# Performance work log

Hardware: AMD Instinct MI355X
Metric: run time of the kernel (lower is better)

Reference implementation:

```python
import jax, jax.numpy as jnp
import numpy as np

L = 16            # number_of_grid_levels
T = 524288        # max_hash_table_entries (2^19)
F = 2             # hash_table_feature_dim
MIN_RES = 16      # coarsest_resolution
MAX_RES = 2048    # finest_resolution
WIDTH = 64        # mlp_width
OUT = 3           # output_channels
N = 1048576       # number of 2D query points
PRIME_Y = np.uint32(2654435761)  # NGP spatial hash prime for dim 1 (dim 0 prime = 1)


def _resolutions():
    g = np.exp((np.log(MAX_RES) - np.log(MIN_RES)) / (L - 1))
    return np.floor(MIN_RES * g ** np.arange(L)).astype(np.float32)  # [L]


def setup_inputs() -> dict:
    key = jax.random.key(0)
    ks = jax.random.split(key, 6)
    x = jax.random.uniform(ks[0], (N, 2), dtype=jnp.float32)
    # NGP hash tables are initialized small uniform
    tables = jax.random.uniform(ks[1], (L, T, F), minval=-1e-4, maxval=1e-4, dtype=jnp.float32)
    def dense(k, fi, fo):
        return (jax.random.normal(k, (fi, fo), dtype=jnp.float32) / np.sqrt(fi).astype(np.float32))
    W0 = dense(ks[2], L * F, WIDTH)
    W1 = dense(ks[3], WIDTH, WIDTH)
    W2 = dense(ks[4], WIDTH, OUT)
    return dict(x=x, tables=tables,
                W0=W0, b0=jnp.zeros((WIDTH,), jnp.float32),
                W1=W1, b1=jnp.zeros((WIDTH,), jnp.float32),
                W2=W2, b2=jnp.zeros((OUT,), jnp.float32))


def _hash_encode(x, tables):
    # Multi-resolution hash grid encoding (Instant-NGP, spatial_dim=2).
    res = jnp.asarray(_resolutions())                  # [L]
    scaled = x[:, None, :] * res[None, :, None]        # [N, L, 2]
    floored = jnp.floor(scaled)
    frac = scaled - floored                            # [N, L, 2]
    corners = jnp.array([[0, 0], [1, 0], [0, 1], [1, 1]], dtype=jnp.int32)  # [4, 2]
    vert = floored.astype(jnp.int32)[:, :, None, :] + corners[None, None]   # [N, L, 4, 2]
    vu = vert.astype(jnp.uint32)
    h = vu[..., 0] ^ (vu[..., 1] * PRIME_Y)            # spatial hash (prime for dim0 is 1)
    idx = (h % jnp.uint32(T)).astype(jnp.int32)        # [N, L, 4]
    feats = tables[jnp.arange(L)[None, :, None], idx]  # [N, L, 4, F] gather per level
    # bilinear weights: prod over dims of frac (if corner==1) else 1-frac
    wd = jnp.where(corners[None, None] == 1, frac[:, :, None, :], 1.0 - frac[:, :, None, :])
    w = wd[..., 0] * wd[..., 1]                        # [N, L, 4]
    interp = jnp.einsum('nlc,nlcf->nlf', w, feats)     # [N, L, F]
    return interp.reshape(x.shape[0], L * F)           # [N, L*F]


def reference(x, tables, W0, b0, W1, b1, W2, b2):
    h = _hash_encode(x, tables)
    h = jax.nn.relu(h @ W0 + b0)
    h = jax.nn.relu(h @ W1 + b1)
    return jax.nn.sigmoid(h @ W2 + b2)   # [N, 3]
```

## Files before the change

kernel.cpp:

```cpp
#include <hip/hip_runtime.h>

#define LVLS  16
#define TSZ   524288u
#define TMASK (TSZ - 1u)
#define PRIME 2654435761u

__constant__ float RES[LVLS] = {16.f, 22.f, 30.f, 42.f, 58.f, 80.f, 111.f, 153.f,
                                212.f, 294.f, 406.f, 561.f, 776.f, 1072.f, 1482.f, 2048.f};

typedef __bf16 bf16x8 __attribute__((ext_vector_type(8)));
typedef float  f32x4  __attribute__((ext_vector_type(4)));

union Frag {
    uint4          q;
    unsigned       u[4];
    unsigned short s[8];
    bf16x8         v;
};

static __device__ __forceinline__ unsigned short f2bf(float f) {
    unsigned u = __float_as_uint(f);
    u += 0x7FFFu + ((u >> 16) & 1u);
    return (unsigned short)(u >> 16);
}
static __device__ __forceinline__ unsigned pack2(float a, float b) {
    return (unsigned)f2bf(a) | ((unsigned)f2bf(b) << 16);
}
static __device__ __forceinline__ void lds_fence() {
    asm volatile("s_waitcnt lgkmcnt(0)" ::: "memory");
}

__global__ __launch_bounds__(256) void ngp_encode(
    const float* __restrict__ x, const float* __restrict__ tables,
    unsigned* __restrict__ feat, int N, int PB)
{
    const int g  = blockIdx.x;
    const int r  = g & 7;
    const int i  = g >> 3;
    const int hi = (i >= PB);
    const int l  = r + (hi << 3);
    const int pb = i - (hi ? PB : 0);
    const int n  = pb * 256 + threadIdx.x;
    if (n >= N) return;

    const float2 xy = ((const float2*)x)[n];
    const float res = RES[l];
    const float sx = xy.x * res, sy = xy.y * res;
    const float fx = floorf(sx),  fy = floorf(sy);
    const float ux = sx - fx,     uy = sy - fy;
    const unsigned ix = (unsigned)(int)fx, iy = (unsigned)(int)fy;
    const unsigned hy0 = iy * PRIME, hy1 = (iy + 1u) * PRIME;
    const unsigned i00 = (ix ^ hy0) & TMASK;
    const unsigned i10 = ((ix + 1u) ^ hy0) & TMASK;
    const unsigned i01 = (ix ^ hy1) & TMASK;
    const unsigned i11 = ((ix + 1u) ^ hy1) & TMASK;
    const float2* tb = (const float2*)(tables + (size_t)l * (TSZ * 2));
    const float2 f00 = tb[i00], f10 = tb[i10], f01 = tb[i01], f11 = tb[i11];
    const float w00 = (1.f - ux) * (1.f - uy);
    const float w10 = ux * (1.f - uy);
    const float w01 = (1.f - ux) * uy;
    const float w11 = ux * uy;
    const float e0 = w00*f00.x + w10*f10.x + w01*f01.x + w11*f11.x;
    const float e1 = w00*f00.y + w10*f10.y + w01*f01.y + w11*f11.y;
    feat[(size_t)l * N + n] = pack2(e0, e1);
}

__global__ __launch_bounds__(256) void ngp_mlp(
    const unsigned* __restrict__ feat,
    const float* __restrict__ W0, const float* __restrict__ b0,
    const float* __restrict__ W1, const float* __restrict__ b1,
    const float* __restrict__ W2, const float* __restrict__ b2,
    float* __restrict__ out, int N)
{
    __shared__ uint4 sB0[4 * 64];
    __shared__ uint4 sB1[8 * 64];
    __shared__ uint4 sB2[2 * 64];
    __shared__ __align__(16) unsigned short hscr[4][16][72];

    const int tid  = threadIdx.x;
    const int lane = tid & 63;
    const int w    = tid >> 6;
    const int c    = lane & 15;
    const int quad = lane >> 4;

    {
        const int f = tid >> 6;
        Frag t0;
        #pragma unroll
        for (int j = 0; j < 8; ++j)
            t0.s[j] = f2bf(W0[(quad * 8 + j) * 64 + f * 16 + c]);
        sB0[f * 64 + lane] = t0.q;

        #pragma unroll
        for (int pass = 0; pass < 2; ++pass) {
            const int ff = f + pass * 4;
            const int kt = ff >> 2, tt = ff & 3;
            Frag t1;
            #pragma unroll
            for (int j = 0; j < 8; ++j)
                t1.s[j] = f2bf(W1[(kt * 32 + quad * 8 + j) * 64 + tt * 16 + c]);
            sB1[ff * 64 + lane] = t1.q;
        }
        if (f < 2) {
            Frag t2;
            #pragma unroll
            for (int j = 0; j < 8; ++j) {
                const float v = (c < 3) ? W2[(f * 32 + quad * 8 + j) * 3 + c] : 0.f;
                t2.s[j] = f2bf(v);
            }
            sB2[f * 64 + lane] = t2.q;
        }
    }
    __syncthreads();

    Frag B0f[4], B1f[8], B2f[2];
    #pragma unroll
    for (int t = 0; t < 4; ++t) B0f[t].q = sB0[t * 64 + lane];
    #pragma unroll
    for (int f = 0; f < 8; ++f) B1f[f].q = sB1[f * 64 + lane];
    #pragma unroll
    for (int f = 0; f < 2; ++f) B2f[f].q = sB2[f * 64 + lane];

    float bias0[4], bias1[4];
    #pragma unroll
    for (int t = 0; t < 4; ++t) { bias0[t] = b0[t * 16 + c]; bias1[t] = b1[t * 16 + c]; }
    const float bias2 = (c < 3) ? b2[c] : 0.f;

    #pragma unroll 1
    for (int it = 0; it < 4; ++it) {
        const int n0 = blockIdx.x * 256 + w * 64 + it * 16;

        Frag a0;
        #pragma unroll
        for (int i = 0; i < 4; ++i)
            a0.u[i] = feat[(size_t)(quad * 4 + i) * N + n0 + c];

        f32x4 acc0[4];
        #pragma unroll
        for (int t = 0; t < 4; ++t) {
            f32x4 cin = {bias0[t], bias0[t], bias0[t], bias0[t]};
            acc0[t] = __builtin_amdgcn_mfma_f32_16x16x32_bf16(a0.v, B0f[t].v, cin, 0, 0, 0);
        }

        lds_fence();
        #pragma unroll
        for (int t = 0; t < 4; ++t)
            #pragma unroll
            for (int rr = 0; rr < 4; ++rr)
                hscr[w][quad * 4 + rr][t * 16 + c] = f2bf(fmaxf(acc0[t][rr], 0.f));

        lds_fence();
        Frag a1[2];
        #pragma unroll
        for (int kt = 0; kt < 2; ++kt)
            a1[kt].q = *(const uint4*)&hscr[w][c][kt * 32 + quad * 8];

        f32x4 acc1[4];
        #pragma unroll
        for (int t = 0; t < 4; ++t) {
            f32x4 cin = {bias1[t], bias1[t], bias1[t], bias1[t]};
            cin = __builtin_amdgcn_mfma_f32_16x16x32_bf16(a1[0].v, B1f[t].v, cin, 0, 0, 0);
            acc1[t] = __builtin_amdgcn_mfma_f32_16x16x32_bf16(a1[1].v, B1f[4 + t].v, cin, 0, 0, 0);
        }

        lds_fence();
        #pragma unroll
        for (int t = 0; t < 4; ++t)
            #pragma unroll
            for (int rr = 0; rr < 4; ++rr)
                hscr[w][quad * 4 + rr][t * 16 + c] = f2bf(fmaxf(acc1[t][rr], 0.f));

        lds_fence();
        Frag a2[2];
        #pragma unroll
        for (int kt = 0; kt < 2; ++kt)
            a2[kt].q = *(const uint4*)&hscr[w][c][kt * 32 + quad * 8];

        f32x4 cin2 = {bias2, bias2, bias2, bias2};
        cin2 = __builtin_amdgcn_mfma_f32_16x16x32_bf16(a2[0].v, B2f[0].v, cin2, 0, 0, 0);
        f32x4 acc2 = __builtin_amdgcn_mfma_f32_16x16x32_bf16(a2[1].v, B2f[1].v, cin2, 0, 0, 0);

        if (c < 3) {
            #pragma unroll
            for (int rr = 0; rr < 4; ++rr) {
                const float s = 1.f / (1.f + __expf(-acc2[rr]));
                out[(size_t)(n0 + quad * 4 + rr) * 3 + c] = s;
            }
        }
    }
}

extern "C" void kernel_launch(void* const* d_in, const int* in_sizes, int n_in,
                              void* d_out, int out_size, void* d_ws, size_t ws_size,
                              hipStream_t stream) {
    const float* x      = (const float*)d_in[0];
    const float* tables = (const float*)d_in[1];
    const float* W0     = (const float*)d_in[2];
    const float* b0     = (const float*)d_in[3];
    const float* W1     = (const float*)d_in[4];
    const float* b1     = (const float*)d_in[5];
    const float* W2     = (const float*)d_in[6];
    const float* b2     = (const float*)d_in[7];
    float* out = (float*)d_out;
    unsigned* feat = (unsigned*)d_ws;

    const int N  = in_sizes[0] / 2;
    const int PB = (N + 255) / 256;
    ngp_encode<<<16 * PB, 256, 0, stream>>>(x, tables, feat, N, PB);
    ngp_mlp<<<PB, 256, 0, stream>>>(feat, W0, b0, W1, b1, W2, b2, out, N);
}
```

Measured before the change: 309.6 us.

## Fuse hash encoding into MLP kernel with LDS feature staging and paired corner loads

Merges the separate encode and MLP kernels into one kernel with 512-thread blocks. Each thread computes all 16 levels for its point and writes the packed bf16 features to a swizzled LDS buffer instead of a global workspace, which removes the feature round trip through HBM. When ix is even, the two x-adjacent corners sit in one aligned 16-byte pair, so each is fetched with a single vector load, halving the gather count on that path. The cost is that the level-major L2 locality of the old per-level grid is lost, since every block now touches all 16 tables, and LDS use rises, which may limit occupancy.

```diff
diff --git a/kernel.cpp b/kernel.cpp
--- a/kernel.cpp
+++ b/kernel.cpp
@@ -30,43 +30,8 @@
     asm volatile("s_waitcnt lgkmcnt(0)" ::: "memory");
 }
 
-__global__ __launch_bounds__(256) void ngp_encode(
+__global__ __launch_bounds__(512, 4) void ngp_fused(
     const float* __restrict__ x, const float* __restrict__ tables,
-    unsigned* __restrict__ feat, int N, int PB)
-{
-    const int g  = blockIdx.x;
-    const int r  = g & 7;
-    const int i  = g >> 3;
-    const int hi = (i >= PB);
-    const int l  = r + (hi << 3);
-    const int pb = i - (hi ? PB : 0);
-    const int n  = pb * 256 + threadIdx.x;
-    if (n >= N) return;
-
-    const float2 xy = ((const float2*)x)[n];
-    const float res = RES[l];
-    const float sx = xy.x * res, sy = xy.y * res;
-    const float fx = floorf(sx),  fy = floorf(sy);
-    const float ux = sx - fx,     uy = sy - fy;
-    const unsigned ix = (unsigned)(int)fx, iy = (unsigned)(int)fy;
-    const unsigned hy0 = iy * PRIME, hy1 = (iy + 1u) * PRIME;
-    const unsigned i00 = (ix ^ hy0) & TMASK;
-    const unsigned i10 = ((ix + 1u) ^ hy0) & TMASK;
-    const unsigned i01 = (ix ^ hy1) & TMASK;
-    const unsigned i11 = ((ix + 1u) ^ hy1) & TMASK;
-    const float2* tb = (const float2*)(tables + (size_t)l * (TSZ * 2));
-    const float2 f00 = tb[i00], f10 = tb[i10], f01 = tb[i01], f11 = tb[i11];
-    const float w00 = (1.f - ux) * (1.f - uy);
-    const float w10 = ux * (1.f - uy);
-    const float w01 = (1.f - ux) * uy;
-    const float w11 = ux * uy;
-    const float e0 = w00*f00.x + w10*f10.x + w01*f01.x + w11*f11.x;
-    const float e1 = w00*f00.y + w10*f10.y + w01*f01.y + w11*f11.y;
-    feat[(size_t)l * N + n] = pack2(e0, e1);
-}
-
-__global__ __launch_bounds__(256) void ngp_mlp(
-    const unsigned* __restrict__ feat,
     const float* __restrict__ W0, const float* __restrict__ b0,
     const float* __restrict__ W1, const float* __restrict__ b1,
     const float* __restrict__ W2, const float* __restrict__ b2,
@@ -74,8 +39,8 @@
 {
     __shared__ uint4 sB0[4 * 64];
     __shared__ uint4 sB1[8 * 64];
-    __shared__ uint4 sB2[2 * 64];
-    __shared__ __align__(16) unsigned short hscr[4][16][72];
+    __shared__ unsigned sfeat[8][LVLS][64];
+    __shared__ __align__(16) unsigned short hscr[8][16][72];
 
     const int tid  = threadIdx.x;
     const int lane = tid & 63;
@@ -84,31 +49,62 @@
     const int quad = lane >> 4;
 
     {
-        const int f = tid >> 6;
-        Frag t0;
-        #pragma unroll
-        for (int j = 0; j < 8; ++j)
-            t0.s[j] = f2bf(W0[(quad * 8 + j) * 64 + f * 16 + c]);
-        sB0[f * 64 + lane] = t0.q;
-
-        #pragma unroll
-        for (int pass = 0; pass < 2; ++pass) {
-            const int ff = f + pass * 4;
-            const int kt = ff >> 2, tt = ff & 3;
+        const int f = w;
+        if (f < 4) {
+            Frag t0;
+            #pragma unroll
+            for (int j = 0; j < 8; ++j)
+                t0.s[j] = f2bf(W0[(quad * 8 + j) * 64 + f * 16 + c]);
+            sB0[f * 64 + lane] = t0.q;
+        }
+        {
+            const int kt = f >> 2, tt = f & 3;
             Frag t1;
             #pragma unroll
             for (int j = 0; j < 8; ++j)
                 t1.s[j] = f2bf(W1[(kt * 32 + quad * 8 + j) * 64 + tt * 16 + c]);
-            sB1[ff * 64 + lane] = t1.q;
-        }
-        if (f < 2) {
-            Frag t2;
-            #pragma unroll
-            for (int j = 0; j < 8; ++j) {
-                const float v = (c < 3) ? W2[(f * 32 + quad * 8 + j) * 3 + c] : 0.f;
-                t2.s[j] = f2bf(v);
+            sB1[f * 64 + lane] = t1.q;
+        }
+    }
+
+    const int n = blockIdx.x * 512 + tid;
+    if (n < N) {
+        const float2 xy = ((const float2*)x)[n];
+        #pragma unroll 4
+        for (int l = 0; l < LVLS; ++l) {
+            const float res = RES[l];
+            const float sx = xy.x * res, sy = xy.y * res;
+            const float fx = floorf(sx),  fy = floorf(sy);
+            const float ux = sx - fx,     uy = sy - fy;
+            const unsigned ix = (unsigned)(int)fx, iy = (unsigned)(int)fy;
+            const unsigned hy0 = iy * PRIME, hy1 = (iy + 1u) * PRIME;
+            const unsigned i00 = (ix ^ hy0) & TMASK;
+            const unsigned i01 = (ix ^ hy1) & TMASK;
+            const float* tbf = tables + (size_t)l * (TSZ * 2u);
+            float2 f00, f10, f01, f11;
+            if (!(ix & 1u)) {
+                const f32x4 a = *(const f32x4*)(tbf + 2u * (i00 & ~1u));
+                const f32x4 b = *(const f32x4*)(tbf + 2u * (i01 & ~1u));
+                const bool s0 = (i00 & 1u) != 0u;
+                const bool s1 = (i01 & 1u) != 0u;
+                f00 = s0 ? make_float2(a[2], a[3]) : make_float2(a[0], a[1]);
+                f10 = s0 ? make_float2(a[0], a[1]) : make_float2(a[2], a[3]);
+                f01 = s1 ? make_float2(b[2], b[3]) : make_float2(b[0], b[1]);
+                f11 = s1 ? make_float2(b[0], b[1]) : make_float2(b[2], b[3]);
+            } else {
+                const unsigned i10 = ((ix + 1u) ^ hy0) & TMASK;
+                const unsigned i11 = ((ix + 1u) ^ hy1) & TMASK;
+                const float2* tb2 = (const float2*)tbf;
+                f00 = tb2[i00]; f10 = tb2[i10];
+                f01 = tb2[i01]; f11 = tb2[i11];
             }
-            sB2[f * 64 + lane] = t2.q;
+            const float w00 = (1.f - ux) * (1.f - uy);
+            const float w10 = ux * (1.f - uy);
+            const float w01 = (1.f - ux) * uy;
+            const float w11 = ux * uy;
+            const float e0 = w00*f00.x + w10*f10.x + w01*f01.x + w11*f11.x;
+            const float e1 = w00*f00.y + w10*f10.y + w01*f01.y + w11*f11.y;
+            sfeat[w][l][lane ^ (((l >> 2) & 3) << 4)] = pack2(e0, e1);
         }
     }
     __syncthreads();
@@ -119,7 +115,13 @@
     #pragma unroll
     for (int f = 0; f < 8; ++f) B1f[f].q = sB1[f * 64 + lane];
     #pragma unroll
-    for (int f = 0; f < 2; ++f) B2f[f].q = sB2[f * 64 + lane];
+    for (int f = 0; f < 2; ++f) {
+        #pragma unroll
+        for (int j = 0; j < 8; ++j) {
+            const float v = (c < 3) ? W2[(f * 32 + quad * 8 + j) * 3 + c] : 0.f;
+            B2f[f].s[j] = f2bf(v);
+        }
+    }
 
     float bias0[4], bias1[4];
     #pragma unroll
@@ -128,12 +130,12 @@
 
     #pragma unroll 1
     for (int it = 0; it < 4; ++it) {
-        const int n0 = blockIdx.x * 256 + w * 64 + it * 16;
+        const int n0 = blockIdx.x * 512 + w * 64 + it * 16;
 
         Frag a0;
         #pragma unroll
         for (int i = 0; i < 4; ++i)
-            a0.u[i] = feat[(size_t)(quad * 4 + i) * N + n0 + c];
+            a0.u[i] = sfeat[w][quad * 4 + i][(it * 16 + c) ^ (quad << 4)];
 
         f32x4 acc0[4];
         #pragma unroll
@@ -183,8 +185,10 @@
         if (c < 3) {
             #pragma unroll
             for (int rr = 0; rr < 4; ++rr) {
-                const float s = 1.f / (1.f + __expf(-acc2[rr]));
-                out[(size_t)(n0 + quad * 4 + rr) * 3 + c] = s;
+                if (n0 + quad * 4 + rr < N) {
+                    const float s = 1.f / (1.f + __expf(-acc2[rr]));
+                    out[(size_t)(n0 + quad * 4 + rr) * 3 + c] = s;
+                }
             }
         }
     }
@@ -202,10 +206,9 @@
     const float* W2     = (const float*)d_in[6];
     const float* b2     = (const float*)d_in[7];
     float* out = (float*)d_out;
-    unsigned* feat = (unsigned*)d_ws;
+    (void)d_ws; (void)ws_size; (void)n_in; (void)out_size;
 
     const int N  = in_sizes[0] / 2;
-    const int PB = (N + 255) / 256;
-    ngp_encode<<<16 * PB, 256, 0, stream>>>(x, tables, feat, N, PB);
-    ngp_mlp<<<PB, 256, 0, stream>>>(feat, W0, b0, W1, b1, W2, b2, out, N);
-}
+    const int PB = (N + 511) / 512;
+    ngp_fused<<<PB, 512, 0, stream>>>(x, tables, W0, b0, W1, b1, W2, b2, out, N);
+}
```

Measured after the change: 271.7 us. 1.14x faster.
